# Optimization experiments

Hardware: AMD Instinct MI355X
Metric: run time of the kernel (lower is better)

Reference implementation:

```python
import jax, jax.numpy as jnp
import numpy as np

B, S, DIM = 2, 2048, 2048
INTER = 1024          # moe_inter_dim
E = 8                 # n_routed_experts
K = 2                 # n_activated_experts
N_SHARED = 1
ROUTE_SCALE = 1.0


def setup_inputs() -> dict:
    key = jax.random.key(0)
    ks = jax.random.split(key, 8)
    s_in = 1.0 / np.sqrt(DIM)
    s_hid = 1.0 / np.sqrt(INTER)
    return {
        "x": jax.random.normal(ks[0], (B, S, DIM), dtype=jnp.float32),
        "gate_w": jax.random.normal(ks[1], (E, DIM), dtype=jnp.float32) * s_in,
        "w1": jax.random.normal(ks[2], (E, INTER, DIM), dtype=jnp.float32) * s_in,
        "w2": jax.random.normal(ks[3], (E, DIM, INTER), dtype=jnp.float32) * s_hid,
        "w3": jax.random.normal(ks[4], (E, INTER, DIM), dtype=jnp.float32) * s_in,
        "ws1": jax.random.normal(ks[5], (N_SHARED * INTER, DIM), dtype=jnp.float32) * s_in,
        "ws2": jax.random.normal(ks[6], (DIM, N_SHARED * INTER), dtype=jnp.float32) * s_hid,
        "ws3": jax.random.normal(ks[7], (N_SHARED * INTER, DIM), dtype=jnp.float32) * s_in,
    }


def reference(x, gate_w, w1, w2, w3, ws1, ws2, ws3):
    shape = x.shape
    xf = x.reshape(-1, DIM)                         # [T, d]
    # --- Gate: softmax scores, top-k (single group => plain top-k) ---
    scores = jax.nn.softmax(xf @ gate_w.T, axis=-1)  # [T, E]
    weights, idx = jax.lax.top_k(scores, K)          # [T, K]
    weights = weights * ROUTE_SCALE
    # --- Routed experts (dense compute + one-hot combine) ---
    h = jnp.einsum('td,eid->eti', xf, w1)            # [E, T, inter]
    g = jax.nn.silu(h) * jnp.einsum('td,eid->eti', xf, w3)
    eo = jnp.einsum('eti,edi->etd', g, w2)           # [E, T, d]
    comb = jnp.einsum('tke,tk->te', jax.nn.one_hot(idx, E, dtype=xf.dtype), weights)
    y = jnp.einsum('etd,te->td', eo, comb)           # [T, d]
    # --- Shared expert MLP (SwiGLU) ---
    z = (jax.nn.silu(xf @ ws1.T) * (xf @ ws3.T)) @ ws2.T
    return (y + z).reshape(shape)
```

## Files before the change

kernel.cpp:

```cpp
#include <hip/hip_runtime.h>
#include <stdint.h>

#define T_TOK 4096
#define DIM   2048
#define INTER 1024
#define NE    9
#define NPAIR 12288

typedef float v4f __attribute__((ext_vector_type(4)));
typedef short v8s __attribute__((ext_vector_type(8)));

__device__ __forceinline__ unsigned short f2bf(float f) {
    unsigned u = __float_as_uint(f);
    u += 0x7fffu + ((u >> 16) & 1u);
    return (unsigned short)(u >> 16);
}

__device__ __forceinline__ void gload_lds16(const void* g, void* l) {
    __builtin_amdgcn_global_load_lds(
        (const __attribute__((address_space(1))) void*)g,
        (__attribute__((address_space(3))) void*)l, 16, 0, 0);
}

__global__ __launch_bounds__(256) void cvt_w_kernel(
        const float* __restrict__ w1,  const float* __restrict__ ws1, unsigned short* __restrict__ w1b,
        const float* __restrict__ w3,  const float* __restrict__ ws3, unsigned short* __restrict__ w3b,
        const float* __restrict__ w2,  const float* __restrict__ ws2, unsigned short* __restrict__ w2b) {
    int which = blockIdx.y;
    const float* wmain = (which == 0) ? w1  : (which == 1) ? w3  : w2;
    const float* wsh   = (which == 0) ? ws1 : (which == 1) ? ws3 : ws2;
    unsigned short* dst = (which == 0) ? w1b : (which == 1) ? w3b : w2b;
    long long i = (long long)blockIdx.x * 256 + threadIdx.x;
    long long base = i * 4;
    int e = (int)(base >> 21);
    long long within = base & ((1ll << 21) - 1);
    const float* src = (e < 8) ? (wmain + ((long long)e << 21) + within) : (wsh + within);
    float4 f = *(const float4*)src;
    ushort4 u;
    u.x = f2bf(f.x); u.y = f2bf(f.y); u.z = f2bf(f.z); u.w = f2bf(f.w);
    *(ushort4*)(dst + base) = u;
}

__global__ __launch_bounds__(256) void gate_kernel(const float* __restrict__ x,
                                                   const float* __restrict__ gw,
                                                   float* __restrict__ wt,
                                                   int* __restrict__ ei,
                                                   unsigned short* __restrict__ xb) {
    __shared__ float xs[DIM];
    __shared__ float lg[8];
    int t = blockIdx.x;
    const float* xrow = x + (size_t)t * DIM;
    for (int i = threadIdx.x; i < DIM / 4; i += 256)
        ((float4*)xs)[i] = ((const float4*)xrow)[i];
    __syncthreads();
    for (int i = threadIdx.x; i < DIM / 4; i += 256) {
        float4 f = ((const float4*)xs)[i];
        ushort4 u;
        u.x = f2bf(f.x); u.y = f2bf(f.y); u.z = f2bf(f.z); u.w = f2bf(f.w);
        ((ushort4*)(xb + (size_t)t * DIM))[i] = u;
    }
    int e = threadIdx.x >> 5;
    int l = threadIdx.x & 31;
    const float* g = gw + (size_t)e * DIM;
    float p = 0.f;
    #pragma unroll 8
    for (int d = l; d < DIM; d += 32) p += xs[d] * g[d];
    for (int m = 16; m >= 1; m >>= 1) p += __shfl_xor(p, m, 32);
    if (l == 0) lg[e] = p;
    __syncthreads();
    if (threadIdx.x == 0) {
        float mx = lg[0];
        for (int i = 1; i < 8; i++) mx = fmaxf(mx, lg[i]);
        float pr[8], s = 0.f;
        for (int i = 0; i < 8; i++) { pr[i] = __expf(lg[i] - mx); s += pr[i]; }
        float inv = 1.f / s;
        float b1 = -1.f, b2 = -1.f; int i1 = 0, i2 = 0;
        for (int i = 0; i < 8; i++) {
            float v = pr[i] * inv;
            if (v > b1)      { b2 = b1; i2 = i1; b1 = v; i1 = i; }
            else if (v > b2) { b2 = v;  i2 = i; }
        }
        wt[t * 3 + 0] = b1; wt[t * 3 + 1] = b2; wt[t * 3 + 2] = 1.f;
        ei[t * 3 + 0] = i1; ei[t * 3 + 1] = i2; ei[t * 3 + 2] = 8;
    }
}

__global__ void zero_meta_kernel(int* meta) {
    if (threadIdx.x < 18) meta[threadIdx.x] = 0;
}
__global__ __launch_bounds__(256) void count_kernel(const int* __restrict__ ei,
                                                    int* __restrict__ meta) {
    __shared__ int lcnt[NE];
    if (threadIdx.x < NE) lcnt[threadIdx.x] = 0;
    __syncthreads();
    int t = blockIdx.x * 256 + threadIdx.x;
    #pragma unroll
    for (int s = 0; s < 3; s++) atomicAdd(&lcnt[ei[t * 3 + s]], 1);
    __syncthreads();
    if (threadIdx.x < NE) atomicAdd(&meta[threadIdx.x], lcnt[threadIdx.x]);
}
__global__ void scan_meta_kernel(int* meta) {
    if (threadIdx.x == 0) {
        int a = 0;
        for (int e = 0; e < NE; e++) { meta[18 + e] = a; a += meta[e]; }
    }
}
__global__ __launch_bounds__(256) void fill_kernel(const int* __restrict__ ei,
                                                   const float* __restrict__ wt,
                                                   int* __restrict__ meta,
                                                   int* __restrict__ pair_tok,
                                                   float* __restrict__ pair_w,
                                                   int* __restrict__ slots) {
    __shared__ int lcnt[NE], lbase[NE];
    if (threadIdx.x < NE) lcnt[threadIdx.x] = 0;
    __syncthreads();
    int t = blockIdx.x * 256 + threadIdx.x;
    int es[3], lp[3];
    #pragma unroll
    for (int s = 0; s < 3; s++) {
        es[s] = ei[t * 3 + s];
        lp[s] = atomicAdd(&lcnt[es[s]], 1);
    }
    __syncthreads();
    if (threadIdx.x < NE)
        lbase[threadIdx.x] = atomicAdd(&meta[9 + threadIdx.x], lcnt[threadIdx.x]);
    __syncthreads();
    #pragma unroll
    for (int s = 0; s < 3; s++) {
        int g = meta[18 + es[s]] + lbase[es[s]] + lp[s];
        pair_tok[g] = t;
        pair_w[g] = wt[t * 3 + s];
        slots[t * 3 + s] = g;
    }
}

__global__ __launch_bounds__(256, 3) void gemm1_kernel(
        const unsigned short* __restrict__ xb,
        const unsigned short* __restrict__ w1b,
        const unsigned short* __restrict__ w3b,
        unsigned short* __restrict__ G,
        const int* __restrict__ meta,
        const int* __restrict__ pair_tok,
        const float* __restrict__ pair_w) {
    int e = blockIdx.z;
    int cnt = meta[e];
    int m0 = blockIdx.y * 128;
    if (m0 >= cnt) return;
    int off = meta[18 + e];
    int n0 = blockIdx.x * 64;

    __shared__ __align__(16) unsigned short As[128 * 64];
    __shared__ __align__(16) unsigned short B1s[64 * 64];
    __shared__ __align__(16) unsigned short B3s[64 * 64];

    int tid = threadIdx.x;
    int wave = tid >> 6, lane = tid & 63;
    int kc = (lane & 7) ^ (lane >> 3);

    const unsigned short* sbase;
    unsigned short* ldst;
    unsigned soff[8];
    if (wave < 2) {
        sbase = xb;
        ldst = As + wave * 4096;
        #pragma unroll
        for (int j = 0; j < 8; j++) {
            int row = (wave * 8 + j) * 8 + (lane >> 3);
            int p = m0 + row; p = p < cnt ? p : cnt - 1;
            int tok = pair_tok[off + p];
            soff[j] = (unsigned)tok * DIM + (unsigned)(kc * 8);
        }
    } else {
        const unsigned short* wsrc = (wave == 2) ? w1b : w3b;
        ldst = (wave == 2) ? B1s : B3s;
        sbase = wsrc + ((size_t)e * INTER + n0 + (lane >> 3)) * DIM + kc * 8;
    }

    int wm = wave >> 1, wn = wave & 1;
    int mb = wm * 64, nb = wn * 32;
    v4f zero4 = {0.f, 0.f, 0.f, 0.f};
    v4f acc1[4][2], acc3[4][2];
    #pragma unroll
    for (int i = 0; i < 4; i++)
        #pragma unroll
        for (int j = 0; j < 2; j++) { acc1[i][j] = zero4; acc3[i][j] = zero4; }

    for (int k0 = 0; k0 < DIM; k0 += 64) {
        if (wave < 2) {
            #pragma unroll
            for (int j = 0; j < 8; j++)
                gload_lds16(sbase + soff[j] + k0, ldst + j * 512);
        } else {
            #pragma unroll
            for (int j = 0; j < 8; j++)
                gload_lds16(sbase + (unsigned)(j * 8 * DIM) + k0, ldst + j * 512);
        }
        __syncthreads();
        #pragma unroll
        for (int s = 0; s < 2; s++) {
            int kk = s * 4 + (lane >> 4);
            v8s a[4], b1[2], b3[2];
            #pragma unroll
            for (int mt = 0; mt < 4; mt++) {
                int r = mb + mt * 16 + (lane & 15);
                a[mt] = *(const v8s*)&As[r * 64 + ((kk ^ (r & 7)) << 3)];
            }
            #pragma unroll
            for (int nt = 0; nt < 2; nt++) {
                int n = nb + nt * 16 + (lane & 15);
                int o = n * 64 + ((kk ^ (n & 7)) << 3);
                b1[nt] = *(const v8s*)&B1s[o];
                b3[nt] = *(const v8s*)&B3s[o];
            }
            #pragma unroll
            for (int mt = 0; mt < 4; mt++)
                #pragma unroll
                for (int nt = 0; nt < 2; nt++) {
                    acc1[mt][nt] = __builtin_amdgcn_mfma_f32_16x16x32_bf16(a[mt], b1[nt], acc1[mt][nt], 0, 0, 0);
                    acc3[mt][nt] = __builtin_amdgcn_mfma_f32_16x16x32_bf16(a[mt], b3[nt], acc3[mt][nt], 0, 0, 0);
                }
        }
        __syncthreads();
    }

    #pragma unroll
    for (int mt = 0; mt < 4; mt++) {
        #pragma unroll
        for (int r = 0; r < 4; r++) {
            int row = mb + mt * 16 + ((lane >> 4) << 2) + r;
            int p = m0 + row;
            if (p < cnt) {
                float w = pair_w[off + p];
                size_t gbase = (size_t)(off + p) * INTER + n0 + nb;
                #pragma unroll
                for (int nt = 0; nt < 2; nt++) {
                    float h1 = acc1[mt][nt][r];
                    float h3 = acc3[mt][nt][r];
                    float gv = h1 / (1.f + __expf(-h1)) * h3 * w;
                    G[gbase + nt * 16 + (lane & 15)] = f2bf(gv);
                }
            }
        }
    }
}

__global__ __launch_bounds__(256, 3) void gemm2_kernel(
        const unsigned short* __restrict__ G,
        const unsigned short* __restrict__ w2b,
        unsigned short* __restrict__ eo,
        const int* __restrict__ meta) {
    int e = blockIdx.z;
    int cnt = meta[e];
    int m0 = blockIdx.y * 128;
    if (m0 >= cnt) return;
    int off = meta[18 + e];
    int n0 = blockIdx.x * 128;

    __shared__ __align__(16) unsigned short As[128 * 64];
    __shared__ __align__(16) unsigned short Bs[128 * 64];

    int tid = threadIdx.x;
    int wave = tid >> 6, lane = tid & 63;
    int kc = (lane & 7) ^ (lane >> 3);

    const unsigned short* sbase;
    unsigned short* ldst;
    unsigned soff[8];
    if (wave < 2) {
        sbase = G;
        ldst = As + wave * 4096;
        #pragma unroll
        for (int j = 0; j < 8; j++) {
            int row = (wave * 8 + j) * 8 + (lane >> 3);
            int p = m0 + row; p = p < cnt ? p : cnt - 1;
            soff[j] = (unsigned)(off + p) * INTER + (unsigned)(kc * 8);
        }
    } else {
        int g0 = (wave - 2) * 64;
        ldst = Bs + (wave - 2) * 4096;
        sbase = w2b + ((size_t)e * DIM + n0 + g0 + (lane >> 3)) * INTER + kc * 8;
    }

    int wm = wave >> 1, wn = wave & 1;
    int mb = wm * 64, nbw = wn * 64;
    v4f zero4 = {0.f, 0.f, 0.f, 0.f};
    v4f acc[4][4];
    #pragma unroll
    for (int i = 0; i < 4; i++)
        #pragma unroll
        for (int j = 0; j < 4; j++) acc[i][j] = zero4;

    for (int k0 = 0; k0 < INTER; k0 += 64) {
        if (wave < 2) {
            #pragma unroll
            for (int j = 0; j < 8; j++)
                gload_lds16(sbase + soff[j] + k0, ldst + j * 512);
        } else {
            #pragma unroll
            for (int j = 0; j < 8; j++)
                gload_lds16(sbase + (unsigned)(j * 8 * INTER) + k0, ldst + j * 512);
        }
        __syncthreads();
        #pragma unroll
        for (int s = 0; s < 2; s++) {
            int kk = s * 4 + (lane >> 4);
            v8s a[4], b[4];
            #pragma unroll
            for (int mt = 0; mt < 4; mt++) {
                int r = mb + mt * 16 + (lane & 15);
                a[mt] = *(const v8s*)&As[r * 64 + ((kk ^ (r & 7)) << 3)];
            }
            #pragma unroll
            for (int nt = 0; nt < 4; nt++) {
                int n = nbw + nt * 16 + (lane & 15);
                b[nt] = *(const v8s*)&Bs[n * 64 + ((kk ^ (n & 7)) << 3)];
            }
            #pragma unroll
            for (int mt = 0; mt < 4; mt++)
                #pragma unroll
                for (int nt = 0; nt < 4; nt++)
                    acc[mt][nt] = __builtin_amdgcn_mfma_f32_16x16x32_bf16(a[mt], b[nt], acc[mt][nt], 0, 0, 0);
        }
        __syncthreads();
    }

    #pragma unroll
    for (int mt = 0; mt < 4; mt++) {
        #pragma unroll
        for (int r = 0; r < 4; r++) {
            int row = mb + mt * 16 + ((lane >> 4) << 2) + r;
            int p = m0 + row;
            if (p < cnt) {
                unsigned short* obase = eo + (size_t)(off + p) * DIM + n0 + nbw;
                #pragma unroll
                for (int nt = 0; nt < 4; nt++)
                    obase[nt * 16 + (lane & 15)] = f2bf(acc[mt][nt][r]);
            }
        }
    }
}

__global__ __launch_bounds__(256) void combine_kernel(const unsigned short* __restrict__ eo,
                                                      const int* __restrict__ slots,
                                                      float* __restrict__ out) {
    int t = blockIdx.x;
    int p0 = slots[t * 3 + 0], p1 = slots[t * 3 + 1], p2 = slots[t * 3 + 2];
    const ushort4* r0 = (const ushort4*)(eo + (size_t)p0 * DIM);
    const ushort4* r1 = (const ushort4*)(eo + (size_t)p1 * DIM);
    const ushort4* r2 = (const ushort4*)(eo + (size_t)p2 * DIM);
    float4* o = (float4*)(out + (size_t)t * DIM);
    for (int i = threadIdx.x; i < DIM / 4; i += 256) {
        ushort4 a = r0[i], b = r1[i], c = r2[i];
        float4 v;
        v.x = __uint_as_float((unsigned)a.x << 16) + __uint_as_float((unsigned)b.x << 16) + __uint_as_float((unsigned)c.x << 16);
        v.y = __uint_as_float((unsigned)a.y << 16) + __uint_as_float((unsigned)b.y << 16) + __uint_as_float((unsigned)c.y << 16);
        v.z = __uint_as_float((unsigned)a.z << 16) + __uint_as_float((unsigned)b.z << 16) + __uint_as_float((unsigned)c.z << 16);
        v.w = __uint_as_float((unsigned)a.w << 16) + __uint_as_float((unsigned)b.w << 16) + __uint_as_float((unsigned)c.w << 16);
        o[i] = v;
    }
}

extern "C" void kernel_launch(void* const* d_in, const int* in_sizes, int n_in,
                              void* d_out, int out_size, void* d_ws, size_t ws_size,
                              hipStream_t stream) {
    const float* x   = (const float*)d_in[0];
    const float* gw  = (const float*)d_in[1];
    const float* w1  = (const float*)d_in[2];
    const float* w2  = (const float*)d_in[3];
    const float* w3  = (const float*)d_in[4];
    const float* ws1 = (const float*)d_in[5];
    const float* ws2 = (const float*)d_in[6];
    const float* ws3 = (const float*)d_in[7];
    float* out = (float*)d_out;

    char* p = (char*)d_ws;
    auto alloc = [&](size_t bytes) {
        void* r = (void*)p;
        p += (bytes + 255) & ~(size_t)255;
        return r;
    };
    unsigned short* xb  = (unsigned short*)alloc((size_t)T_TOK * DIM * 2);
    unsigned short* w1b = (unsigned short*)alloc((size_t)NE * INTER * DIM * 2);
    unsigned short* w3b = (unsigned short*)alloc((size_t)NE * INTER * DIM * 2);
    unsigned short* w2b = (unsigned short*)alloc((size_t)NE * DIM * INTER * 2);
    unsigned short* G   = (unsigned short*)alloc((size_t)NPAIR * INTER * 2);
    int*   ei    = (int*)alloc((size_t)T_TOK * 3 * 4);
    float* wt    = (float*)alloc((size_t)T_TOK * 3 * 4);
    int*   ptok  = (int*)alloc((size_t)NPAIR * 4);
    float* pw    = (float*)alloc((size_t)NPAIR * 4);
    int*   slots = (int*)alloc((size_t)NPAIR * 4);
    int*   meta  = (int*)alloc(32 * 4);
    unsigned short* eo = w1b;

    zero_meta_kernel<<<1, 32, 0, stream>>>(meta);
    int wgrid = (NE * INTER * DIM / 4) / 256;
    cvt_w_kernel<<<dim3(wgrid, 3), 256, 0, stream>>>(w1, ws1, w1b, w3, ws3, w3b, w2, ws2, w2b);
    gate_kernel<<<T_TOK, 256, 0, stream>>>(x, gw, wt, ei, xb);
    count_kernel<<<T_TOK / 256, 256, 0, stream>>>(ei, meta);
    scan_meta_kernel<<<1, 1, 0, stream>>>(meta);
    fill_kernel<<<T_TOK / 256, 256, 0, stream>>>(ei, wt, meta, ptok, pw, slots);
    gemm1_kernel<<<dim3(INTER / 64, 32, NE), 256, 0, stream>>>(xb, w1b, w3b, G, meta, ptok, pw);
    gemm2_kernel<<<dim3(DIM / 128, 32, NE), 256, 0, stream>>>(G, w2b, eo, meta);
    combine_kernel<<<T_TOK, 256, 0, stream>>>(eo, slots, out);
}
```

Measured before the change: 463.8 us.

## Fold w2 conversion into gemm1 spare blocks and drop tiny meta kernels

The fp32-to-bf16 conversion of w2/ws2 moves out of the standalone convert kernel and into extra blocks of the gemm1 launch, so it runs alongside the expert GEMM. The meta zeroing moves into the w1/w3 conversion kernel. The prefix-sum scan kernel is removed, with offsets now recomputed inline in fill and the GEMMs. This cuts two tiny launches and aims to overlap memory-bound conversion with compute, at the cost of the converting blocks competing with GEMM blocks for CU slots and bandwidth.

```diff
diff --git a/kernel.cpp b/kernel.cpp
--- a/kernel.cpp
+++ b/kernel.cpp
@@ -22,14 +22,15 @@
         (__attribute__((address_space(3))) void*)l, 16, 0, 0);
 }
 
-__global__ __launch_bounds__(256) void cvt_w_kernel(
+__global__ __launch_bounds__(256) void cvt_w13_kernel(
         const float* __restrict__ w1,  const float* __restrict__ ws1, unsigned short* __restrict__ w1b,
         const float* __restrict__ w3,  const float* __restrict__ ws3, unsigned short* __restrict__ w3b,
-        const float* __restrict__ w2,  const float* __restrict__ ws2, unsigned short* __restrict__ w2b) {
+        int* __restrict__ meta) {
+    if (blockIdx.x == 0 && blockIdx.y == 0 && threadIdx.x < 18) meta[threadIdx.x] = 0;
     int which = blockIdx.y;
-    const float* wmain = (which == 0) ? w1  : (which == 1) ? w3  : w2;
-    const float* wsh   = (which == 0) ? ws1 : (which == 1) ? ws3 : ws2;
-    unsigned short* dst = (which == 0) ? w1b : (which == 1) ? w3b : w2b;
+    const float* wmain = (which == 0) ? w1  : w3;
+    const float* wsh   = (which == 0) ? ws1 : ws3;
+    unsigned short* dst = (which == 0) ? w1b : w3b;
     long long i = (long long)blockIdx.x * 256 + threadIdx.x;
     long long base = i * 4;
     int e = (int)(base >> 21);
@@ -85,9 +86,6 @@
     }
 }
 
-__global__ void zero_meta_kernel(int* meta) {
-    if (threadIdx.x < 18) meta[threadIdx.x] = 0;
-}
 __global__ __launch_bounds__(256) void count_kernel(const int* __restrict__ ei,
                                                     int* __restrict__ meta) {
     __shared__ int lcnt[NE];
@@ -99,19 +97,14 @@
     __syncthreads();
     if (threadIdx.x < NE) atomicAdd(&meta[threadIdx.x], lcnt[threadIdx.x]);
 }
-__global__ void scan_meta_kernel(int* meta) {
-    if (threadIdx.x == 0) {
-        int a = 0;
-        for (int e = 0; e < NE; e++) { meta[18 + e] = a; a += meta[e]; }
-    }
-}
+
 __global__ __launch_bounds__(256) void fill_kernel(const int* __restrict__ ei,
                                                    const float* __restrict__ wt,
                                                    int* __restrict__ meta,
                                                    int* __restrict__ pair_tok,
                                                    float* __restrict__ pair_w,
                                                    int* __restrict__ slots) {
-    __shared__ int lcnt[NE], lbase[NE];
+    __shared__ int lcnt[NE], lbase[NE], loffs[NE];
     if (threadIdx.x < NE) lcnt[threadIdx.x] = 0;
     __syncthreads();
     int t = blockIdx.x * 256 + threadIdx.x;
@@ -124,10 +117,15 @@
     __syncthreads();
     if (threadIdx.x < NE)
         lbase[threadIdx.x] = atomicAdd(&meta[9 + threadIdx.x], lcnt[threadIdx.x]);
+    if (threadIdx.x == 0) {
+        int a = 0;
+        #pragma unroll
+        for (int e = 0; e < NE; e++) { loffs[e] = a; a += meta[e]; }
+    }
     __syncthreads();
     #pragma unroll
     for (int s = 0; s < 3; s++) {
-        int g = meta[18 + es[s]] + lbase[es[s]] + lp[s];
+        int g = loffs[es[s]] + lbase[es[s]] + lp[s];
         pair_tok[g] = t;
         pair_w[g] = wt[t * 3 + s];
         slots[t * 3 + s] = g;
@@ -141,12 +139,33 @@
         unsigned short* __restrict__ G,
         const int* __restrict__ meta,
         const int* __restrict__ pair_tok,
-        const float* __restrict__ pair_w) {
+        const float* __restrict__ pair_w,
+        const float* __restrict__ w2f,
+        const float* __restrict__ ws2,
+        unsigned short* __restrict__ w2b) {
+    if (blockIdx.y >= 32) {
+        int flat = (blockIdx.z * 8 + (blockIdx.y - 32)) * 16 + blockIdx.x;
+        long long vbase = (long long)flat * 4096 + threadIdx.x;
+        #pragma unroll
+        for (int it = 0; it < 16; ++it) {
+            long long i = vbase + it * 256;
+            long long base = i * 4;
+            int e = (int)(base >> 21);
+            long long within = base & ((1ll << 21) - 1);
+            const float* src = (e < 8) ? (w2f + ((long long)e << 21) + within) : (ws2 + within);
+            float4 f = *(const float4*)src;
+            ushort4 u;
+            u.x = f2bf(f.x); u.y = f2bf(f.y); u.z = f2bf(f.z); u.w = f2bf(f.w);
+            *(ushort4*)(w2b + base) = u;
+        }
+        return;
+    }
     int e = blockIdx.z;
     int cnt = meta[e];
     int m0 = blockIdx.y * 128;
     if (m0 >= cnt) return;
-    int off = meta[18 + e];
+    int off = 0;
+    for (int i = 0; i < e; i++) off += meta[i];
     int n0 = blockIdx.x * 64;
 
     __shared__ __align__(16) unsigned short As[128 * 64];
@@ -253,7 +272,8 @@
     int cnt = meta[e];
     int m0 = blockIdx.y * 128;
     if (m0 >= cnt) return;
-    int off = meta[18 + e];
+    int off = 0;
+    for (int i = 0; i < e; i++) off += meta[i];
     int n0 = blockIdx.x * 128;
 
     __shared__ __align__(16) unsigned short As[128 * 64];
@@ -392,14 +412,13 @@
     int*   meta  = (int*)alloc(32 * 4);
     unsigned short* eo = w1b;
 
-    zero_meta_kernel<<<1, 32, 0, stream>>>(meta);
     int wgrid = (NE * INTER * DIM / 4) / 256;
-    cvt_w_kernel<<<dim3(wgrid, 3), 256, 0, stream>>>(w1, ws1, w1b, w3, ws3, w3b, w2, ws2, w2b);
+    cvt_w13_kernel<<<dim3(wgrid, 2), 256, 0, stream>>>(w1, ws1, w1b, w3, ws3, w3b, meta);
     gate_kernel<<<T_TOK, 256, 0, stream>>>(x, gw, wt, ei, xb);
     count_kernel<<<T_TOK / 256, 256, 0, stream>>>(ei, meta);
-    scan_meta_kernel<<<1, 1, 0, stream>>>(meta);
     fill_kernel<<<T_TOK / 256, 256, 0, stream>>>(ei, wt, meta, ptok, pw, slots);
-    gemm1_kernel<<<dim3(INTER / 64, 32, NE), 256, 0, stream>>>(xb, w1b, w3b, G, meta, ptok, pw);
+    gemm1_kernel<<<dim3(INTER / 64, 40, NE), 256, 0, stream>>>(xb, w1b, w3b, G, meta, ptok, pw,
+                                                               w2, ws2, w2b);
     gemm2_kernel<<<dim3(DIM / 128, 32, NE), 256, 0, stream>>>(G, w2b, eo, meta);
     combine_kernel<<<T_TOK, 256, 0, stream>>>(eo, slots, out);
 }
```

Result: faster. 445.0 us (-4.1%).
